# Optimization experiments

Hardware: AMD Instinct MI355X
Metric: run time of the kernel (lower is better)

Reference implementation:

```python
import jax, jax.numpy as jnp
import numpy as np

B, H, W, C = 8, 64, 64, 512
C8, C2 = C // 8, C // 2  # f/g channels = 64, h channels = 256 (divisor = 2)


def _maxpool2x2(t):
    # [B, H, W, F] -> [B, H//2, W//2, F], valid 2x2 max pooling
    b, h, w, f = t.shape
    return t.reshape(b, h // 2, 2, w // 2, 2, f).max(axis=(2, 4))


def setup_inputs() -> dict:
    key = jax.random.key(0)
    kx, kf, kg, kh, ko, kgam = jax.random.split(key, 6)
    sf = lambda fan_in: (1.0 / np.sqrt(fan_in)).astype(np.float32)
    return {
        "x": jax.random.normal(kx, (B, H, W, C), dtype=jnp.float32),
        "wf": jax.random.normal(kf, (C, C8), dtype=jnp.float32) * sf(C),
        "wg": jax.random.normal(kg, (C, C8), dtype=jnp.float32) * sf(C),
        "wh": jax.random.normal(kh, (C, C2), dtype=jnp.float32) * sf(C),
        "wo": jax.random.normal(ko, (C2, C), dtype=jnp.float32) * sf(C2),
        "gamma": jax.random.normal(kgam, (1,), dtype=jnp.float32) * 0.1,
    }


def reference(x, wf, wg, wh, wo, gamma):
    b = x.shape[0]
    # 1x1 convs == channel matmuls
    f = _maxpool2x2(jnp.einsum("bhwc,cd->bhwd", x, wf)).reshape(b, -1, C8)  # [B, N/4, C/8]
    g = jnp.einsum("bhwc,cd->bhwd", x, wg).reshape(b, -1, C8)               # [B, N,   C/8]
    s = jnp.einsum("bqd,bkd->bqk", g, f)                                     # unscaled scores
    beta = jax.nn.softmax(s, axis=-1)
    h = _maxpool2x2(jnp.einsum("bhwc,cd->bhwd", x, wh)).reshape(b, -1, C2)  # [B, N/4, C/2]
    o = jnp.einsum("bqk,bkd->bqd", beta, h).reshape(b, H, W, C2)
    o = jnp.einsum("bhwd,dc->bhwc", o, wo)                                   # o_conv back to C
    return gamma * o + x
```

## Files before the change

### kernel.cpp

```cpp
#include <hip/hip_runtime.h>
#include <hip/hip_bf16.h>

#define NTOK 4096
#define NPOOL 1024

using short8 = __attribute__((ext_vector_type(8))) short;
using f32x4  = __attribute__((ext_vector_type(4))) float;

__device__ __forceinline__ unsigned short f2bf(float f) {
  __hip_bfloat16 h = __float2bfloat16(f);
  return __builtin_bit_cast(unsigned short, h);
}

__device__ __forceinline__ int pool_row(int bx, int m) {
  int pg = bx * 16 + (m >> 2);
  int corner = m & 3;
  int batch = pg >> 10;
  int pl = pg & 1023;
  int pi = pl >> 5, pj = pl & 31;
  return (batch << 12) + ((2 * pi + (corner >> 1)) << 6) + 2 * pj + (corner & 1);
}

__global__ __launch_bounds__(256) void pack_w(const float* __restrict__ wf,
                                              const float* __restrict__ wg,
                                              const float* __restrict__ wh,
                                              const float* __restrict__ wo,
                                              unsigned short* __restrict__ wcatT,
                                              unsigned short* __restrict__ woT) {
  int i = blockIdx.x * 256 + threadIdx.x;
  if (i < 384 * 512) {
    int n = i >> 9, k = i & 511;
    float v = (n < 64) ? wf[k * 64 + n]
            : (n < 128) ? wg[k * 64 + (n - 64)]
                        : wh[k * 256 + (n - 128)];
    wcatT[i] = f2bf(v);
  } else if (i < 384 * 512 + 512 * 256) {
    int j = i - 384 * 512;
    int n = j >> 8, k = j & 255;
    woT[j] = f2bf(wo[(size_t)k * 512 + n]);
  }
}

__global__ __launch_bounds__(256) void fgh_proj(const float* __restrict__ x,
                                                const unsigned short* __restrict__ wcatT,
                                                unsigned short* __restrict__ fB,
                                                unsigned short* __restrict__ gB,
                                                unsigned short* __restrict__ hT) {
  __shared__ unsigned short lds[17920];
  const int tid = threadIdx.x;
  const int bx = blockIdx.x;
  const int wave = tid >> 6, lane = tid & 63;
  const int col = lane & 15, rgrp = lane >> 4;

  f32x4 acc[4][6];
#pragma unroll
  for (int mt = 0; mt < 4; ++mt)
#pragma unroll
    for (int nt = 0; nt < 6; ++nt) acc[mt][nt] = (f32x4){0.f, 0.f, 0.f, 0.f};

  for (int kt = 0; kt < 16; ++kt) {
    __syncthreads();
#pragma unroll
    for (int r = 0; r < 2; ++r) {
      int idx = tid + r * 256;
      int m = idx >> 3, k4 = (idx & 7) << 2;
      float4 v = *(const float4*)(x + (size_t)pool_row(bx, m) * 512 + kt * 32 + k4);
      ushort4 o4;
      o4.x = f2bf(v.x); o4.y = f2bf(v.y); o4.z = f2bf(v.z); o4.w = f2bf(v.w);
      *(ushort4*)&lds[m * 40 + k4] = o4;
    }
#pragma unroll
    for (int r = 0; r < 6; ++r) {
      int idx = tid + r * 256;
      int n = idx >> 2, k8 = (idx & 3) << 3;
      *(uint4*)&lds[2560 + n * 40 + k8] =
          *(const uint4*)(wcatT + (size_t)n * 512 + kt * 32 + k8);
    }
    __syncthreads();

    short8 am[4];
#pragma unroll
    for (int mt = 0; mt < 4; ++mt)
      am[mt] = *(const short8*)&lds[(mt * 16 + col) * 40 + rgrp * 8];
#pragma unroll
    for (int nt = 0; nt < 6; ++nt) {
      short8 bn = *(const short8*)&lds[2560 + (wave * 96 + nt * 16 + col) * 40 + rgrp * 8];
#pragma unroll
      for (int mt = 0; mt < 4; ++mt)
        acc[mt][nt] = __builtin_amdgcn_mfma_f32_16x16x32_bf16(am[mt], bn, acc[mt][nt], 0, 0, 0);
    }
  }
  __syncthreads();

  unsigned short* gO = lds;
  unsigned short* fO = lds + 4608;
  unsigned short* hO = lds + 5760;
#pragma unroll
  for (int mt = 0; mt < 4; ++mt) {
#pragma unroll
    for (int nt = 0; nt < 6; ++nt) {
      int n = wave * 96 + nt * 16 + col;
      f32x4 a = acc[mt][nt];
      if (n < 64) {
        float mx = fmaxf(fmaxf(a[0], a[1]), fmaxf(a[2], a[3]));
        fO[(mt * 4 + rgrp) * 72 + n] = f2bf(mx);
      } else if (n < 128) {
#pragma unroll
        for (int reg = 0; reg < 4; ++reg)
          gO[(mt * 16 + rgrp * 4 + reg) * 72 + (n - 64)] = f2bf(a[reg]);
      } else {
        float mx = fmaxf(fmaxf(a[0], a[1]), fmaxf(a[2], a[3]));
        hO[(n - 128) * 24 + (mt * 4 + rgrp)] = f2bf(mx);
      }
    }
  }
  __syncthreads();

  const int b = bx >> 6, pkb = (bx & 63) * 16;
#pragma unroll
  for (int r = 0; r < 2; ++r) {
    int idx = tid + r * 256;
    int m = idx >> 3, d8 = (idx & 7) << 3;
    *(uint4*)(gB + (size_t)pool_row(bx, m) * 64 + d8) = *(const uint4*)&gO[m * 72 + d8];
  }
  if (tid < 128) {
    int pr = tid >> 3, d8 = (tid & 7) << 3;
    *(uint4*)(fB + (size_t)(bx * 16 + pr) * 64 + d8) = *(const uint4*)&fO[pr * 72 + d8];
  }
#pragma unroll
  for (int r = 0; r < 2; ++r) {
    int idx = tid + r * 256;
    int dv = idx >> 1, p8 = (idx & 1) << 3;
    *(uint4*)(hT + (((size_t)b * 256 + dv) << 10) + pkb + p8) = *(const uint4*)&hO[dv * 24 + p8];
  }
}

__global__ __launch_bounds__(256) void attn_mfma(const __hip_bfloat16* __restrict__ G,
                                                 const __hip_bfloat16* __restrict__ F,
                                                 const __hip_bfloat16* __restrict__ HT,
                                                 unsigned short* __restrict__ O) {
  __shared__ __hip_bfloat16 gS[64][72];
  __shared__ __hip_bfloat16 fS[64][72];
  __shared__ __hip_bfloat16 hS[256][72];
  __shared__ __hip_bfloat16 pS[64][72];

  const int tid = threadIdx.x;
  const int wave = tid >> 6, lane = tid & 63;
  const int col = lane & 15;
  const int rgrp = lane >> 4;
  const int b = blockIdx.x >> 6, qt = blockIdx.x & 63;

  const __hip_bfloat16* Gb = G + ((size_t)b * NTOK + qt * 64) * 64;
  const __hip_bfloat16* Fb = F + (size_t)b * NPOOL * 64;
  const __hip_bfloat16* Hb = HT + (size_t)b * 256 * NPOOL;

#pragma unroll
  for (int r = 0; r < 2; ++r) {
    int j = tid + r * 256;
    int q = j >> 3, d8 = (j & 7) << 3;
    *(uint4*)&gS[q][d8] = *(const uint4*)(Gb + (size_t)q * 64 + d8);
  }
  __syncthreads();

  short8 ag[2];
#pragma unroll
  for (int ks = 0; ks < 2; ++ks)
    ag[ks] = *(const short8*)&gS[wave * 16 + col][ks * 32 + rgrp * 8];

  f32x4 oacc[16];
#pragma unroll
  for (int t = 0; t < 16; ++t) oacc[t] = (f32x4){0.f, 0.f, 0.f, 0.f};
  float m_run[4], l_run[4];
#pragma unroll
  for (int r = 0; r < 4; ++r) { m_run[r] = -1e30f; l_run[r] = 0.f; }

  for (int kc = 0; kc < 16; ++kc) {
    __syncthreads();
#pragma unroll
    for (int r = 0; r < 2; ++r) {
      int j = tid + r * 256;
      int k = j >> 3, d8 = (j & 7) << 3;
      *(uint4*)&fS[k][d8] = *(const uint4*)(Fb + (size_t)(kc * 64 + k) * 64 + d8);
    }
#pragma unroll
    for (int r = 0; r < 8; ++r) {
      int j = tid + r * 256;
      int dv = j >> 3, k8 = (j & 7) << 3;
      *(uint4*)&hS[dv][k8] = *(const uint4*)(Hb + (size_t)dv * NPOOL + kc * 64 + k8);
    }
    __syncthreads();

    f32x4 s[4];
#pragma unroll
    for (int t = 0; t < 4; ++t) s[t] = (f32x4){0.f, 0.f, 0.f, 0.f};
#pragma unroll
    for (int ks = 0; ks < 2; ++ks) {
#pragma unroll
      for (int t = 0; t < 4; ++t) {
        short8 bf = *(const short8*)&fS[t * 16 + col][ks * 32 + rgrp * 8];
        s[t] = __builtin_amdgcn_mfma_f32_16x16x32_bf16(ag[ks], bf, s[t], 0, 0, 0);
      }
    }

    float cm[4];
#pragma unroll
    for (int r = 0; r < 4; ++r) {
      cm[r] = fmaxf(fmaxf(s[0][r], s[1][r]), fmaxf(s[2][r], s[3][r]));
#pragma unroll
      for (int msk = 1; msk < 16; msk <<= 1) cm[r] = fmaxf(cm[r], __shfl_xor(cm[r], msk));
    }
    float alpha[4], rs[4];
#pragma unroll
    for (int r = 0; r < 4; ++r) {
      float mn = fmaxf(m_run[r], cm[r]);
      alpha[r] = __expf(m_run[r] - mn);
      m_run[r] = mn;
      rs[r] = 0.f;
    }
    const int prow = wave * 16 + rgrp * 4;
#pragma unroll
    for (int t = 0; t < 4; ++t) {
#pragma unroll
      for (int r = 0; r < 4; ++r) {
        float p = __expf(s[t][r] - m_run[r]);
        rs[r] += p;
        pS[prow + r][t * 16 + col] = __float2bfloat16(p);
      }
    }
#pragma unroll
    for (int r = 0; r < 4; ++r) {
#pragma unroll
      for (int msk = 1; msk < 16; msk <<= 1) rs[r] += __shfl_xor(rs[r], msk);
      l_run[r] = alpha[r] * l_run[r] + rs[r];
    }

#pragma unroll
    for (int t = 0; t < 16; ++t) {
#pragma unroll
      for (int r = 0; r < 4; ++r) oacc[t][r] *= alpha[r];
    }

    short8 ap[2];
#pragma unroll
    for (int ks = 0; ks < 2; ++ks)
      ap[ks] = *(const short8*)&pS[wave * 16 + col][ks * 32 + rgrp * 8];
#pragma unroll
    for (int t = 0; t < 16; ++t) {
#pragma unroll
      for (int ks = 0; ks < 2; ++ks) {
        short8 bh = *(const short8*)&hS[t * 16 + col][ks * 32 + rgrp * 8];
        oacc[t] = __builtin_amdgcn_mfma_f32_16x16x32_bf16(ap[ks], bh, oacc[t], 0, 0, 0);
      }
    }
  }

  float inv[4];
#pragma unroll
  for (int r = 0; r < 4; ++r) inv[r] = 1.0f / l_run[r];
  __syncthreads();
  unsigned short* oS = (unsigned short*)&hS[0][0];
  const int qrow = wave * 16 + rgrp * 4;
#pragma unroll
  for (int t = 0; t < 16; ++t) {
#pragma unroll
    for (int r = 0; r < 4; ++r)
      oS[(qrow + r) * 264 + t * 16 + col] = f2bf(oacc[t][r] * inv[r]);
  }
  __syncthreads();
  unsigned short* Ob = O + ((size_t)b * NTOK + qt * 64) * 256;
#pragma unroll
  for (int r = 0; r < 8; ++r) {
    int idx = tid + r * 256;
    int q = idx >> 5, d8 = (idx & 31) << 3;
    *(uint4*)(Ob + (size_t)q * 256 + d8) = *(const uint4*)&oS[q * 264 + d8];
  }
}

__global__ __launch_bounds__(256) void gemm_out_mfma(const unsigned short* __restrict__ Obf,
                                                     const unsigned short* __restrict__ woT,
                                                     const float* __restrict__ Xres,
                                                     const float* __restrict__ gamma,
                                                     float* __restrict__ Out) {
  __shared__ unsigned short lds[23040];
  const int tid = threadIdx.x;
  const int bx = blockIdx.x;
  const int wave = tid >> 6, lane = tid & 63;
  const int col = lane & 15, rgrp = lane >> 4;

  f32x4 acc[4][8];
#pragma unroll
  for (int mt = 0; mt < 4; ++mt)
#pragma unroll
    for (int nt = 0; nt < 8; ++nt) acc[mt][nt] = (f32x4){0.f, 0.f, 0.f, 0.f};

  for (int kt = 0; kt < 8; ++kt) {
    __syncthreads();
    {
      int m = tid >> 2, k8 = (tid & 3) << 3;
      *(uint4*)&lds[m * 40 + k8] =
          *(const uint4*)(Obf + ((size_t)bx * 64 + m) * 256 + kt * 32 + k8);
    }
#pragma unroll
    for (int r = 0; r < 8; ++r) {
      int idx = tid + r * 256;
      int n = idx >> 2, k8 = (idx & 3) << 3;
      *(uint4*)&lds[2560 + n * 40 + k8] =
          *(const uint4*)(woT + (size_t)n * 256 + kt * 32 + k8);
    }
    __syncthreads();

    short8 am[4];
#pragma unroll
    for (int mt = 0; mt < 4; ++mt)
      am[mt] = *(const short8*)&lds[(mt * 16 + col) * 40 + rgrp * 8];
#pragma unroll
    for (int nt = 0; nt < 8; ++nt) {
      short8 bn = *(const short8*)&lds[2560 + (wave * 128 + nt * 16 + col) * 40 + rgrp * 8];
#pragma unroll
      for (int mt = 0; mt < 4; ++mt)
        acc[mt][nt] = __builtin_amdgcn_mfma_f32_16x16x32_bf16(am[mt], bn, acc[mt][nt], 0, 0, 0);
    }
  }

  float gm = gamma[0];
#pragma unroll
  for (int mt = 0; mt < 4; ++mt) {
#pragma unroll
    for (int nt = 0; nt < 8; ++nt) {
      int n = wave * 128 + nt * 16 + col;
#pragma unroll
      for (int reg = 0; reg < 4; ++reg) {
        size_t row = (size_t)bx * 64 + mt * 16 + rgrp * 4 + reg;
        size_t off = row * 512 + n;
        Out[off] = gm * acc[mt][nt][reg] + Xres[off];
      }
    }
  }
}

extern "C" void kernel_launch(void* const* d_in, const int* in_sizes, int n_in,
                              void* d_out, int out_size, void* d_ws, size_t ws_size,
                              hipStream_t stream) {
  (void)in_sizes; (void)n_in; (void)out_size; (void)ws_size;
  const float* x     = (const float*)d_in[0];
  const float* wf    = (const float*)d_in[1];
  const float* wg    = (const float*)d_in[2];
  const float* wh    = (const float*)d_in[3];
  const float* wo    = (const float*)d_in[4];
  const float* gamma = (const float*)d_in[5];
  float* out = (float*)d_out;

  unsigned short* ws = (unsigned short*)d_ws;
  unsigned short* oB    = ws;
  unsigned short* gB    = ws + 8388608;
  unsigned short* fB    = ws + 10485760;
  unsigned short* hT    = ws + 11010048;
  unsigned short* wcatT = ws + 13107200;
  unsigned short* woT   = ws + 13303808;

  dim3 blk(256);
  pack_w<<<1280, blk, 0, stream>>>(wf, wg, wh, wo, wcatT, woT);
  fgh_proj<<<512, blk, 0, stream>>>(x, wcatT, fB, gB, hT);
  attn_mfma<<<512, blk, 0, stream>>>((const __hip_bfloat16*)gB, (const __hip_bfloat16*)fB,
                                     (const __hip_bfloat16*)hT, oB);
  gemm_out_mfma<<<512, blk, 0, stream>>>(oB, woT, x, gamma, out);
}
```

Measured before the change: 262.4 us.

## Register-prefetch next tiles in all GEMM kernels and skip unneeded softmax rescale

In the projection, attention and output GEMM kernels, each thread now loads the next K-tile from global memory into registers while MFMAs run on the current LDS tile, so global load latency overlaps with compute. The attention kernel also reads its G fragment straight from global memory instead of staging it through LDS. It rescales the output accumulator and running sum only when some lane's row maximum grows, which is checked with a wave vote. The cost is higher register pressure, which could lower occupancy in the register-heavy attention kernel.

After: 354.3 us. +35.0%, slower.

```diff
diff --git a/kernel.cpp b/kernel.cpp
--- a/kernel.cpp
+++ b/kernel.cpp
@@ -52,6 +52,31 @@
   const int wave = tid >> 6, lane = tid & 63;
   const int col = lane & 15, rgrp = lane >> 4;
 
+  const float* xsrc[2];
+  int xdst[2];
+#pragma unroll
+  for (int r = 0; r < 2; ++r) {
+    int idx = tid + r * 256;
+    int m = idx >> 3, k4 = (idx & 7) << 2;
+    xsrc[r] = x + (size_t)pool_row(bx, m) * 512 + k4;
+    xdst[r] = m * 40 + k4;
+  }
+  int wsoff[6], wdst[6];
+#pragma unroll
+  for (int r = 0; r < 6; ++r) {
+    int idx = tid + r * 256;
+    int n = idx >> 2, k8 = (idx & 3) << 3;
+    wsoff[r] = n * 512 + k8;
+    wdst[r] = 2560 + n * 40 + k8;
+  }
+
+  float4 rx[2];
+  uint4 rw[6];
+#pragma unroll
+  for (int r = 0; r < 2; ++r) rx[r] = *(const float4*)(xsrc[r]);
+#pragma unroll
+  for (int r = 0; r < 6; ++r) rw[r] = *(const uint4*)(wcatT + wsoff[r]);
+
   f32x4 acc[4][6];
 #pragma unroll
   for (int mt = 0; mt < 4; ++mt)
@@ -62,21 +87,21 @@
     __syncthreads();
 #pragma unroll
     for (int r = 0; r < 2; ++r) {
-      int idx = tid + r * 256;
-      int m = idx >> 3, k4 = (idx & 7) << 2;
-      float4 v = *(const float4*)(x + (size_t)pool_row(bx, m) * 512 + kt * 32 + k4);
       ushort4 o4;
-      o4.x = f2bf(v.x); o4.y = f2bf(v.y); o4.z = f2bf(v.z); o4.w = f2bf(v.w);
-      *(ushort4*)&lds[m * 40 + k4] = o4;
-    }
-#pragma unroll
-    for (int r = 0; r < 6; ++r) {
-      int idx = tid + r * 256;
-      int n = idx >> 2, k8 = (idx & 3) << 3;
-      *(uint4*)&lds[2560 + n * 40 + k8] =
-          *(const uint4*)(wcatT + (size_t)n * 512 + kt * 32 + k8);
-    }
-    __syncthreads();
+      o4.x = f2bf(rx[r].x); o4.y = f2bf(rx[r].y);
+      o4.z = f2bf(rx[r].z); o4.w = f2bf(rx[r].w);
+      *(ushort4*)&lds[xdst[r]] = o4;
+    }
+#pragma unroll
+    for (int r = 0; r < 6; ++r) *(uint4*)&lds[wdst[r]] = rw[r];
+    __syncthreads();
+
+    if (kt < 15) {
+#pragma unroll
+      for (int r = 0; r < 2; ++r) rx[r] = *(const float4*)(xsrc[r] + (kt + 1) * 32);
+#pragma unroll
+      for (int r = 0; r < 6; ++r) rw[r] = *(const uint4*)(wcatT + wsoff[r] + (kt + 1) * 32);
+    }
 
     short8 am[4];
 #pragma unroll
@@ -139,7 +164,6 @@
                                                  const __hip_bfloat16* __restrict__ F,
                                                  const __hip_bfloat16* __restrict__ HT,
                                                  unsigned short* __restrict__ O) {
-  __shared__ __hip_bfloat16 gS[64][72];
   __shared__ __hip_bfloat16 fS[64][72];
   __shared__ __hip_bfloat16 hS[256][72];
   __shared__ __hip_bfloat16 pS[64][72];
@@ -150,22 +174,37 @@
   const int rgrp = lane >> 4;
   const int b = blockIdx.x >> 6, qt = blockIdx.x & 63;
 
-  const __hip_bfloat16* Gb = G + ((size_t)b * NTOK + qt * 64) * 64;
-  const __hip_bfloat16* Fb = F + (size_t)b * NPOOL * 64;
-  const __hip_bfloat16* Hb = HT + (size_t)b * 256 * NPOOL;
-
+  const unsigned short* Gb = (const unsigned short*)G + ((size_t)b * NTOK + qt * 64) * 64;
+  const unsigned short* Fb = (const unsigned short*)F + (size_t)b * NPOOL * 64;
+  const unsigned short* Hb = (const unsigned short*)HT + (size_t)b * 256 * NPOOL;
+
+  short8 ag[2];
+#pragma unroll
+  for (int ks = 0; ks < 2; ++ks)
+    ag[ks] = *(const short8*)(Gb + (size_t)(wave * 16 + col) * 64 + ks * 32 + rgrp * 8);
+
+  int fsoff[2], fdoff[2];
 #pragma unroll
   for (int r = 0; r < 2; ++r) {
     int j = tid + r * 256;
-    int q = j >> 3, d8 = (j & 7) << 3;
-    *(uint4*)&gS[q][d8] = *(const uint4*)(Gb + (size_t)q * 64 + d8);
-  }
-  __syncthreads();
-
-  short8 ag[2];
-#pragma unroll
-  for (int ks = 0; ks < 2; ++ks)
-    ag[ks] = *(const short8*)&gS[wave * 16 + col][ks * 32 + rgrp * 8];
+    int k = j >> 3, d8 = (j & 7) << 3;
+    fsoff[r] = k * 64 + d8;
+    fdoff[r] = k * 72 + d8;
+  }
+  int hsoff[8], hdoff[8];
+#pragma unroll
+  for (int r = 0; r < 8; ++r) {
+    int j = tid + r * 256;
+    int dv = j >> 3, k8 = (j & 7) << 3;
+    hsoff[r] = dv * NPOOL + k8;
+    hdoff[r] = dv * 72 + k8;
+  }
+
+  uint4 rf[2], rh[8];
+#pragma unroll
+  for (int r = 0; r < 2; ++r) rf[r] = *(const uint4*)(Fb + fsoff[r]);
+#pragma unroll
+  for (int r = 0; r < 8; ++r) rh[r] = *(const uint4*)(Hb + hsoff[r]);
 
   f32x4 oacc[16];
 #pragma unroll
@@ -174,21 +213,23 @@
 #pragma unroll
   for (int r = 0; r < 4; ++r) { m_run[r] = -1e30f; l_run[r] = 0.f; }
 
+  unsigned short* fBase = (unsigned short*)&fS[0][0];
+  unsigned short* hBase = (unsigned short*)&hS[0][0];
+
   for (int kc = 0; kc < 16; ++kc) {
     __syncthreads();
 #pragma unroll
-    for (int r = 0; r < 2; ++r) {
-      int j = tid + r * 256;
-      int k = j >> 3, d8 = (j & 7) << 3;
-      *(uint4*)&fS[k][d8] = *(const uint4*)(Fb + (size_t)(kc * 64 + k) * 64 + d8);
-    }
-#pragma unroll
-    for (int r = 0; r < 8; ++r) {
-      int j = tid + r * 256;
-      int dv = j >> 3, k8 = (j & 7) << 3;
-      *(uint4*)&hS[dv][k8] = *(const uint4*)(Hb + (size_t)dv * NPOOL + kc * 64 + k8);
-    }
-    __syncthreads();
+    for (int r = 0; r < 2; ++r) *(uint4*)(fBase + fdoff[r]) = rf[r];
+#pragma unroll
+    for (int r = 0; r < 8; ++r) *(uint4*)(hBase + hdoff[r]) = rh[r];
+    __syncthreads();
+
+    if (kc < 15) {
+#pragma unroll
+      for (int r = 0; r < 2; ++r) rf[r] = *(const uint4*)(Fb + fsoff[r] + (kc + 1) * 4096);
+#pragma unroll
+      for (int r = 0; r < 8; ++r) rh[r] = *(const uint4*)(Hb + hsoff[r] + (kc + 1) * 64);
+    }
 
     f32x4 s[4];
 #pragma unroll
@@ -209,14 +250,26 @@
 #pragma unroll
       for (int msk = 1; msk < 16; msk <<= 1) cm[r] = fmaxf(cm[r], __shfl_xor(cm[r], msk));
     }
-    float alpha[4], rs[4];
-#pragma unroll
-    for (int r = 0; r < 4; ++r) {
-      float mn = fmaxf(m_run[r], cm[r]);
-      alpha[r] = __expf(m_run[r] - mn);
-      m_run[r] = mn;
-      rs[r] = 0.f;
-    }
+    bool upd = false;
+#pragma unroll
+    for (int r = 0; r < 4; ++r) upd |= (cm[r] > m_run[r]);
+    if (__any(upd)) {
+      float alpha[4];
+#pragma unroll
+      for (int r = 0; r < 4; ++r) {
+        float mn = fmaxf(m_run[r], cm[r]);
+        alpha[r] = __expf(m_run[r] - mn);
+        m_run[r] = mn;
+        l_run[r] *= alpha[r];
+      }
+#pragma unroll
+      for (int t = 0; t < 16; ++t) {
+#pragma unroll
+        for (int r = 0; r < 4; ++r) oacc[t][r] *= alpha[r];
+      }
+    }
+
+    float rs[4] = {0.f, 0.f, 0.f, 0.f};
     const int prow = wave * 16 + rgrp * 4;
 #pragma unroll
     for (int t = 0; t < 4; ++t) {
@@ -231,13 +284,7 @@
     for (int r = 0; r < 4; ++r) {
 #pragma unroll
       for (int msk = 1; msk < 16; msk <<= 1) rs[r] += __shfl_xor(rs[r], msk);
-      l_run[r] = alpha[r] * l_run[r] + rs[r];
-    }
-
-#pragma unroll
-    for (int t = 0; t < 16; ++t) {
-#pragma unroll
-      for (int r = 0; r < 4; ++r) oacc[t][r] *= alpha[r];
+      l_run[r] += rs[r];
     }
 
     short8 ap[2];
@@ -287,6 +334,25 @@
   const int wave = tid >> 6, lane = tid & 63;
   const int col = lane & 15, rgrp = lane >> 4;
 
+  const int am_ = tid >> 2, ak8 = (tid & 3) << 3;
+  const int asoff = am_ * 256 + ak8;
+  const int adst = am_ * 40 + ak8;
+  const unsigned short* Ab = Obf + (size_t)bx * 64 * 256;
+
+  int bsoff[8], bdst[8];
+#pragma unroll
+  for (int r = 0; r < 8; ++r) {
+    int idx = tid + r * 256;
+    int n = idx >> 2, k8 = (idx & 3) << 3;
+    bsoff[r] = n * 256 + k8;
+    bdst[r] = 2560 + n * 40 + k8;
+  }
+
+  uint4 rA = *(const uint4*)(Ab + asoff);
+  uint4 rB[8];
+#pragma unroll
+  for (int r = 0; r < 8; ++r) rB[r] = *(const uint4*)(woT + bsoff[r]);
+
   f32x4 acc[4][8];
 #pragma unroll
   for (int mt = 0; mt < 4; ++mt)
@@ -295,19 +361,16 @@
 
   for (int kt = 0; kt < 8; ++kt) {
     __syncthreads();
-    {
-      int m = tid >> 2, k8 = (tid & 3) << 3;
-      *(uint4*)&lds[m * 40 + k8] =
-          *(const uint4*)(Obf + ((size_t)bx * 64 + m) * 256 + kt * 32 + k8);
-    }
-#pragma unroll
-    for (int r = 0; r < 8; ++r) {
-      int idx = tid + r * 256;
-      int n = idx >> 2, k8 = (idx & 3) << 3;
-      *(uint4*)&lds[2560 + n * 40 + k8] =
-          *(const uint4*)(woT + (size_t)n * 256 + kt * 32 + k8);
-    }
-    __syncthreads();
+    *(uint4*)&lds[adst] = rA;
+#pragma unroll
+    for (int r = 0; r < 8; ++r) *(uint4*)&lds[bdst[r]] = rB[r];
+    __syncthreads();
+
+    if (kt < 7) {
+      rA = *(const uint4*)(Ab + asoff + (kt + 1) * 32);
+#pragma unroll
+      for (int r = 0; r < 8; ++r) rB[r] = *(const uint4*)(woT + bsoff[r] + (kt + 1) * 32);
+    }
 
     short8 am[4];
 #pragma unroll
```

## Widen attention blocks to 128 queries, share K/V tiles, skip unneeded rescaling

Applied to the files above, without the earlier changes.

The attention kernel now runs 512-thread blocks that each cover 128 query rows, so every F/H tile loaded into LDS is reused by twice as many waves and the grid halves to 256 blocks. G fragments are read straight from global memory instead of being staged through LDS, and the LDS buffers are merged into one aliased array. The online softmax skips rescaling the accumulator and row sum when no row maximum in the wave rises. The costs are fewer blocks (256 for the device's CUs), a larger LDS footprint per block, and a wave-divergent branch.

Measured after the change: 228.4 us. 13.0% less time.

```diff
diff --git a/kernel.cpp b/kernel.cpp
--- a/kernel.cpp
+++ b/kernel.cpp
@@ -135,37 +135,26 @@
   }
 }
 
-__global__ __launch_bounds__(256) void attn_mfma(const __hip_bfloat16* __restrict__ G,
+__global__ __launch_bounds__(512) void attn_mfma(const __hip_bfloat16* __restrict__ G,
                                                  const __hip_bfloat16* __restrict__ F,
                                                  const __hip_bfloat16* __restrict__ HT,
                                                  unsigned short* __restrict__ O) {
-  __shared__ __hip_bfloat16 gS[64][72];
-  __shared__ __hip_bfloat16 fS[64][72];
-  __shared__ __hip_bfloat16 hS[256][72];
-  __shared__ __hip_bfloat16 pS[64][72];
+  __shared__ unsigned short lds[33792];
 
   const int tid = threadIdx.x;
   const int wave = tid >> 6, lane = tid & 63;
   const int col = lane & 15;
   const int rgrp = lane >> 4;
-  const int b = blockIdx.x >> 6, qt = blockIdx.x & 63;
-
-  const __hip_bfloat16* Gb = G + ((size_t)b * NTOK + qt * 64) * 64;
-  const __hip_bfloat16* Fb = F + (size_t)b * NPOOL * 64;
-  const __hip_bfloat16* Hb = HT + (size_t)b * 256 * NPOOL;
-
-#pragma unroll
-  for (int r = 0; r < 2; ++r) {
-    int j = tid + r * 256;
-    int q = j >> 3, d8 = (j & 7) << 3;
-    *(uint4*)&gS[q][d8] = *(const uint4*)(Gb + (size_t)q * 64 + d8);
-  }
-  __syncthreads();
+  const int b = blockIdx.x >> 5, qt = blockIdx.x & 31;
+
+  const unsigned short* Gb = (const unsigned short*)G + ((size_t)b * NTOK + qt * 128) * 64;
+  const unsigned short* Fb = (const unsigned short*)F + (size_t)b * NPOOL * 64;
+  const unsigned short* Hb = (const unsigned short*)HT + (size_t)b * 256 * NPOOL;
 
   short8 ag[2];
 #pragma unroll
   for (int ks = 0; ks < 2; ++ks)
-    ag[ks] = *(const short8*)&gS[wave * 16 + col][ks * 32 + rgrp * 8];
+    ag[ks] = *(const short8*)(Gb + (size_t)(wave * 16 + col) * 64 + ks * 32 + rgrp * 8);
 
   f32x4 oacc[16];
 #pragma unroll
@@ -174,19 +163,18 @@
 #pragma unroll
   for (int r = 0; r < 4; ++r) { m_run[r] = -1e30f; l_run[r] = 0.f; }
 
+  const int fk = tid >> 3, fd8 = (tid & 7) << 3;
+
   for (int kc = 0; kc < 16; ++kc) {
     __syncthreads();
-#pragma unroll
-    for (int r = 0; r < 2; ++r) {
-      int j = tid + r * 256;
-      int k = j >> 3, d8 = (j & 7) << 3;
-      *(uint4*)&fS[k][d8] = *(const uint4*)(Fb + (size_t)(kc * 64 + k) * 64 + d8);
-    }
-#pragma unroll
-    for (int r = 0; r < 8; ++r) {
-      int j = tid + r * 256;
+    *(uint4*)&lds[fk * 72 + fd8] =
+        *(const uint4*)(Fb + (size_t)(kc * 64 + fk) * 64 + fd8);
+#pragma unroll
+    for (int r = 0; r < 4; ++r) {
+      int j = tid + r * 512;
       int dv = j >> 3, k8 = (j & 7) << 3;
-      *(uint4*)&hS[dv][k8] = *(const uint4*)(Hb + (size_t)dv * NPOOL + kc * 64 + k8);
+      *(uint4*)&lds[4608 + dv * 72 + k8] =
+          *(const uint4*)(Hb + (size_t)dv * NPOOL + kc * 64 + k8);
     }
     __syncthreads();
 
@@ -197,7 +185,7 @@
     for (int ks = 0; ks < 2; ++ks) {
 #pragma unroll
       for (int t = 0; t < 4; ++t) {
-        short8 bf = *(const short8*)&fS[t * 16 + col][ks * 32 + rgrp * 8];
+        short8 bf = *(const short8*)&lds[(t * 16 + col) * 72 + ks * 32 + rgrp * 8];
         s[t] = __builtin_amdgcn_mfma_f32_16x16x32_bf16(ag[ks], bf, s[t], 0, 0, 0);
       }
     }
@@ -209,14 +197,26 @@
 #pragma unroll
       for (int msk = 1; msk < 16; msk <<= 1) cm[r] = fmaxf(cm[r], __shfl_xor(cm[r], msk));
     }
-    float alpha[4], rs[4];
-#pragma unroll
-    for (int r = 0; r < 4; ++r) {
-      float mn = fmaxf(m_run[r], cm[r]);
-      alpha[r] = __expf(m_run[r] - mn);
-      m_run[r] = mn;
-      rs[r] = 0.f;
-    }
+    bool upd = false;
+#pragma unroll
+    for (int r = 0; r < 4; ++r) upd |= (cm[r] > m_run[r]);
+    if (__any(upd)) {
+      float alpha[4];
+#pragma unroll
+      for (int r = 0; r < 4; ++r) {
+        float mn = fmaxf(m_run[r], cm[r]);
+        alpha[r] = __expf(m_run[r] - mn);
+        m_run[r] = mn;
+        l_run[r] *= alpha[r];
+      }
+#pragma unroll
+      for (int t = 0; t < 16; ++t) {
+#pragma unroll
+        for (int r = 0; r < 4; ++r) oacc[t][r] *= alpha[r];
+      }
+    }
+
+    float rs[4] = {0.f, 0.f, 0.f, 0.f};
     const int prow = wave * 16 + rgrp * 4;
 #pragma unroll
     for (int t = 0; t < 4; ++t) {
@@ -224,31 +224,25 @@
       for (int r = 0; r < 4; ++r) {
         float p = __expf(s[t][r] - m_run[r]);
         rs[r] += p;
-        pS[prow + r][t * 16 + col] = __float2bfloat16(p);
+        lds[23040 + (prow + r) * 72 + t * 16 + col] = f2bf(p);
       }
     }
 #pragma unroll
     for (int r = 0; r < 4; ++r) {
 #pragma unroll
       for (int msk = 1; msk < 16; msk <<= 1) rs[r] += __shfl_xor(rs[r], msk);
-      l_run[r] = alpha[r] * l_run[r] + rs[r];
-    }
-
+      l_run[r] += rs[r];
+    }
+
+    short8 ap[2];
+#pragma unroll
+    for (int ks = 0; ks < 2; ++ks)
+      ap[ks] = *(const short8*)&lds[23040 + (wave * 16 + col) * 72 + ks * 32 + rgrp * 8];
 #pragma unroll
     for (int t = 0; t < 16; ++t) {
 #pragma unroll
-      for (int r = 0; r < 4; ++r) oacc[t][r] *= alpha[r];
-    }
-
-    short8 ap[2];
-#pragma unroll
-    for (int ks = 0; ks < 2; ++ks)
-      ap[ks] = *(const short8*)&pS[wave * 16 + col][ks * 32 + rgrp * 8];
-#pragma unroll
-    for (int t = 0; t < 16; ++t) {
-#pragma unroll
       for (int ks = 0; ks < 2; ++ks) {
-        short8 bh = *(const short8*)&hS[t * 16 + col][ks * 32 + rgrp * 8];
+        short8 bh = *(const short8*)&lds[4608 + (t * 16 + col) * 72 + ks * 32 + rgrp * 8];
         oacc[t] = __builtin_amdgcn_mfma_f32_16x16x32_bf16(ap[ks], bh, oacc[t], 0, 0, 0);
       }
     }
@@ -258,21 +252,20 @@
 #pragma unroll
   for (int r = 0; r < 4; ++r) inv[r] = 1.0f / l_run[r];
   __syncthreads();
-  unsigned short* oS = (unsigned short*)&hS[0][0];
   const int qrow = wave * 16 + rgrp * 4;
 #pragma unroll
   for (int t = 0; t < 16; ++t) {
 #pragma unroll
     for (int r = 0; r < 4; ++r)
-      oS[(qrow + r) * 264 + t * 16 + col] = f2bf(oacc[t][r] * inv[r]);
+      lds[(qrow + r) * 264 + t * 16 + col] = f2bf(oacc[t][r] * inv[r]);
   }
   __syncthreads();
-  unsigned short* Ob = O + ((size_t)b * NTOK + qt * 64) * 256;
+  unsigned short* Ob = O + ((size_t)b * NTOK + qt * 128) * 256;
 #pragma unroll
   for (int r = 0; r < 8; ++r) {
-    int idx = tid + r * 256;
+    int idx = tid + r * 512;
     int q = idx >> 5, d8 = (idx & 31) << 3;
-    *(uint4*)(Ob + (size_t)q * 256 + d8) = *(const uint4*)&oS[q * 264 + d8];
+    *(uint4*)(Ob + (size_t)q * 256 + d8) = *(const uint4*)&lds[q * 264 + d8];
   }
 }
 
@@ -361,7 +354,7 @@
   dim3 blk(256);
   pack_w<<<1280, blk, 0, stream>>>(wf, wg, wh, wo, wcatT, woT);
   fgh_proj<<<512, blk, 0, stream>>>(x, wcatT, fB, gB, hT);
-  attn_mfma<<<512, blk, 0, stream>>>((const __hip_bfloat16*)gB, (const __hip_bfloat16*)fB,
-                                     (const __hip_bfloat16*)hT, oB);
+  attn_mfma<<<256, dim3(512), 0, stream>>>((const __hip_bfloat16*)gB, (const __hip_bfloat16*)fB,
+                                           (const __hip_bfloat16*)hT, oB);
   gemm_out_mfma<<<512, blk, 0, stream>>>(oB, woT, x, gamma, out);
 }
```
